# Optimization experiments

Hardware: AMD Instinct MI355X
Metric: run time of the kernel (lower is better)

The kernel has to match this reference:

```python
import jax, jax.numpy as jnp
import numpy as np

N_ENT = 100000
N_REL = 237
IN_DIM = 128
OUT_DIM = 128
E = 400000


def setup_inputs() -> dict:
    key = jax.random.key(0)
    k1, k2, k3, k4, k5, k6, k7, k8 = jax.random.split(key, 8)
    src = jax.random.randint(k1, (E,), 0, N_ENT)
    dst = jax.random.randint(k2, (E,), 0, N_ENT)
    rel = jax.random.randint(k3, (E,), 0, N_REL)
    triplets = jnp.stack([src, dst, rel], axis=1)  # [E, 3]
    ent_embed = jax.random.normal(k4, (N_ENT, IN_DIM), dtype=jnp.float32)
    rel_embed = jax.random.normal(k5, (N_REL, IN_DIM), dtype=jnp.float32)
    # xavier_normal with gain=1.414 for weights; torch Linear bias ~ U(-1/sqrt(fan_in), 1/sqrt(fan_in))
    g = 1.414
    Wa = jax.random.normal(k6, (OUT_DIM, 3 * IN_DIM), dtype=jnp.float32) * (g * np.sqrt(2.0 / (3 * IN_DIM + OUT_DIM)))
    ba = jnp.zeros((OUT_DIM,), dtype=jnp.float32)
    Wa2 = jax.random.normal(k7, (1, OUT_DIM), dtype=jnp.float32) * (g * np.sqrt(2.0 / (OUT_DIM + 1)))
    ba2 = jnp.zeros((1,), dtype=jnp.float32)
    return {"triplets": triplets, "ent_embed": ent_embed, "rel_embed": rel_embed,
            "Wa": Wa, "ba": ba, "Wa2": Wa2, "ba2": ba2}


def reference(triplets, ent_embed, rel_embed, Wa, ba, Wa2, ba2):
    src, dst, rel = triplets[:, 0], triplets[:, 1], triplets[:, 2]
    # per-edge feature: [E, 3*in_dim]
    h = jnp.concatenate([ent_embed[src], rel_embed[rel], ent_embed[dst]], axis=1)
    c = h @ Wa.T + ba                                  # [E, out_dim]
    b = jax.nn.leaky_relu(c @ Wa2.T + ba2)             # [E, 1], slope 0.01
    e_b = jnp.exp(b)                                   # [E, 1]
    # segment-sum over source nodes (torch.sparse.sum over dim=1 of [N,N,F])
    e_b_sum = jax.ops.segment_sum(e_b, src, num_segments=N_ENT)       # [N, 1]
    temp1 = e_b * c                                    # [E, out_dim]
    h_sum = jax.ops.segment_sum(temp1, src, num_segments=N_ENT)       # [N, out_dim]
    ebs = jnp.where(e_b_sum == 0, 1e-12, e_b_sum)
    h_ent = h_sum / ebs                                # [N, out_dim]
    # scatter-mean of temp1 by relation id
    rel_sum = jax.ops.segment_sum(temp1, rel, num_segments=N_REL)     # [R, out_dim]
    rel_cnt = jax.ops.segment_sum(jnp.ones((temp1.shape[0], 1), temp1.dtype), rel, num_segments=N_REL)
    h_rel = rel_sum / jnp.maximum(rel_cnt, 1.0)        # [R, out_dim]
    return jax.nn.elu(h_ent), jax.nn.elu(h_rel)
```

## Files before the change

### kernel.cpp

```cpp
#include <hip/hip_runtime.h>
#include <math.h>

#define N_ENT 100000
#define N_REL 237
#define DIM   128
#define NE    400000


__global__ void k_transpose_wa(const float* __restrict__ Wa, float* __restrict__ WaT) {
    int i = blockIdx.x * 256 + threadIdx.x;
    if (i < 384 * 128) {
        int k = i >> 7, j = i & 127;
        WaT[i] = Wa[j * 384 + k];
    }
}

__global__ void k_proj_rel(const float* __restrict__ rel_e, const float* __restrict__ Wa,
                           const float* __restrict__ ba, float* __restrict__ Pr) {
    int i = blockIdx.x * 256 + threadIdx.x;
    if (i >= N_REL * DIM) return;
    int r = i >> 7, j = i & 127;
    float acc = ba[j];
    const float* wrow = Wa + j * 384 + 128;
    const float* erow = rel_e + r * DIM;
    #pragma unroll 8
    for (int k = 0; k < DIM; ++k) acc += erow[k] * wrow[k];
    Pr[i] = acc;
}

#define KC 16
__global__ __launch_bounds__(256) void k_proj_ent(const float* __restrict__ ent,
        const float* __restrict__ WaT, float* __restrict__ Ps, float* __restrict__ Pd) {
    __shared__ float tile[64 * 132];
    __shared__ float wsh[2 * KC * 128];
    const int tid = threadIdx.x;
    const int row0 = blockIdx.x * 64;

    for (int i = tid; i < 64 * 32; i += 256) {
        int r = i >> 5, c4 = i & 31;
        float4 v = make_float4(0.f, 0.f, 0.f, 0.f);
        if (row0 + r < N_ENT) v = *(const float4*)(ent + (size_t)(row0 + r) * DIM + c4 * 4);
        *(float4*)(tile + r * 132 + c4 * 4) = v;
    }

    const int rg = tid >> 4, cg = tid & 15;
    const int r0 = rg * 4, j0 = cg * 8;

    float accs[4][8], accd[4][8];
    #pragma unroll
    for (int i = 0; i < 4; ++i)
        #pragma unroll
        for (int j = 0; j < 8; ++j) { accs[i][j] = 0.f; accd[i][j] = 0.f; }

    for (int kc = 0; kc < DIM; kc += KC) {
        __syncthreads();
        for (int i = tid; i < KC * 32; i += 256) {
            int kk = i >> 5, c4 = i & 31;
            *(float4*)(wsh + kk * 128 + c4 * 4) =
                *(const float4*)(WaT + (kc + kk) * 128 + c4 * 4);
            *(float4*)(wsh + KC * 128 + kk * 128 + c4 * 4) =
                *(const float4*)(WaT + (256 + kc + kk) * 128 + c4 * 4);
        }
        __syncthreads();
        #pragma unroll
        for (int kk = 0; kk < KC; ++kk) {
            float4 a0 = *(float4*)(wsh + kk * 128 + j0);
            float4 a1 = *(float4*)(wsh + kk * 128 + j0 + 4);
            float4 b0 = *(float4*)(wsh + KC * 128 + kk * 128 + j0);
            float4 b1 = *(float4*)(wsh + KC * 128 + kk * 128 + j0 + 4);
            float ws[8] = {a0.x, a0.y, a0.z, a0.w, a1.x, a1.y, a1.z, a1.w};
            float wd[8] = {b0.x, b0.y, b0.z, b0.w, b1.x, b1.y, b1.z, b1.w};
            #pragma unroll
            for (int i = 0; i < 4; ++i) {
                float e = tile[(r0 + i) * 132 + kc + kk];
                #pragma unroll
                for (int j = 0; j < 8; ++j) {
                    accs[i][j] += e * ws[j];
                    accd[i][j] += e * wd[j];
                }
            }
        }
    }

    #pragma unroll
    for (int i = 0; i < 4; ++i) {
        int row = row0 + r0 + i;
        if (row < N_ENT) {
            float4 o;
            o = make_float4(accs[i][0], accs[i][1], accs[i][2], accs[i][3]);
            *(float4*)(Ps + (size_t)row * DIM + j0) = o;
            o = make_float4(accs[i][4], accs[i][5], accs[i][6], accs[i][7]);
            *(float4*)(Ps + (size_t)row * DIM + j0 + 4) = o;
            o = make_float4(accd[i][0], accd[i][1], accd[i][2], accd[i][3]);
            *(float4*)(Pd + (size_t)row * DIM + j0) = o;
            o = make_float4(accd[i][4], accd[i][5], accd[i][6], accd[i][7]);
            *(float4*)(Pd + (size_t)row * DIM + j0 + 4) = o;
        }
    }
}

__global__ void k_hist2(const int* __restrict__ trip, int* __restrict__ scnt,
                        int* __restrict__ rcnt) {
    __shared__ int lh[N_REL];
    for (int i = threadIdx.x; i < N_REL; i += 256) lh[i] = 0;
    __syncthreads();
    int e0 = blockIdx.x * 1024 + threadIdx.x * 4;
    #pragma unroll
    for (int k = 0; k < 4; ++k) {
        int e = e0 + k;
        if (e < NE) {
            atomicAdd(scnt + trip[3 * e], 1);
            atomicAdd(&lh[trip[3 * e + 2]], 1);
        }
    }
    __syncthreads();
    for (int i = threadIdx.x; i < N_REL; i += 256)
        if (lh[i]) atomicAdd(rcnt + i, lh[i]);
}

__global__ void k_scan1(const int* __restrict__ cnt, int* __restrict__ escan,
                        int* __restrict__ bsum) {
    __shared__ int sh[256];
    const int t = threadIdx.x;
    int base = blockIdx.x * 1024 + t * 4;
    int v[4]; int s = 0;
    #pragma unroll
    for (int k = 0; k < 4; ++k) { int idx = base + k; v[k] = (idx < N_ENT) ? cnt[idx] : 0; s += v[k]; }
    sh[t] = s; __syncthreads();
    for (int off = 1; off < 256; off <<= 1) {
        int u = (t >= off) ? sh[t - off] : 0;
        __syncthreads();
        sh[t] += u;
        __syncthreads();
    }
    int run = sh[t] - s;
    #pragma unroll
    for (int k = 0; k < 4; ++k) { int idx = base + k; if (idx < N_ENT) escan[idx] = run; run += v[k]; }
    if (t == 255) bsum[blockIdx.x] = sh[255];
}

__global__ void k_scan2(int* __restrict__ bsum) {
    __shared__ int sh[128];
    const int t = threadIdx.x;
    int v = (t < 98) ? bsum[t] : 0;
    sh[t] = v; __syncthreads();
    for (int off = 1; off < 128; off <<= 1) {
        int u = (t >= off) ? sh[t - off] : 0;
        __syncthreads();
        sh[t] += u;
        __syncthreads();
    }
    if (t < 98) bsum[t] = sh[t] - v;
}

__global__ void k_scan3(int* __restrict__ row_start, const int* __restrict__ bsum,
                        int* __restrict__ cursor) {
    int i = blockIdx.x * 256 + threadIdx.x;
    if (i < N_ENT) {
        int v = row_start[i] + bsum[i >> 10];
        row_start[i] = v;
        cursor[i] = v;
    } else if (i == N_ENT) {
        row_start[N_ENT] = NE;
    }
}

__global__ void k_relscan(const int* __restrict__ rcnt, int* __restrict__ rrow,
                          int* __restrict__ rcursor) {
    __shared__ int sh[256];
    const int t = threadIdx.x;
    int v = (t < N_REL) ? rcnt[t] : 0;
    sh[t] = v; __syncthreads();
    for (int off = 1; off < 256; off <<= 1) {
        int u = (t >= off) ? sh[t - off] : 0;
        __syncthreads();
        sh[t] += u;
        __syncthreads();
    }
    int excl = sh[t] - v;
    if (t <= N_REL) rrow[t] = excl;
    if (t < N_REL) rcursor[t] = excl;
}

__global__ __launch_bounds__(256) void k_scatter3(const int* __restrict__ trip,
        int* __restrict__ scursor, int* __restrict__ rcursor,
        int* __restrict__ sdst, int* __restrict__ srel,
        int* __restrict__ rsrc, int* __restrict__ rdst) {
    __shared__ int lh[N_REL];
    __shared__ int lbase[N_REL];
    const int t = threadIdx.x;
    for (int i = t; i < N_REL; i += 256) lh[i] = 0;
    __syncthreads();

    const int e0 = blockIdx.x * 1024 + t * 4;
    int sv[4], dv[4], rv[4];
    #pragma unroll
    for (int k = 0; k < 4; ++k) {
        int e = e0 + k;
        if (e < NE) {
            sv[k] = trip[3 * e]; dv[k] = trip[3 * e + 1]; rv[k] = trip[3 * e + 2];
            atomicAdd(&lh[rv[k]], 1);
        } else { sv[k] = -1; }
    }
    __syncthreads();
    for (int i = t; i < N_REL; i += 256) {
        int c = lh[i];
        lbase[i] = c ? atomicAdd(rcursor + i, c) : 0;
        lh[i] = 0;
    }
    __syncthreads();
    #pragma unroll
    for (int k = 0; k < 4; ++k) {
        if (sv[k] >= 0) {
            int p1 = atomicAdd(scursor + sv[k], 1);
            sdst[p1] = dv[k];
            srel[p1] = rv[k];
            int intra = atomicAdd(&lh[rv[k]], 1);
            int p2 = lbase[rv[k]] + intra;
            rsrc[p2] = sv[k];
            rdst[p2] = dv[k];
        }
    }
}

__global__ __launch_bounds__(256) void k_seg(const int* __restrict__ row_start,
        const int* __restrict__ sdst, const int* __restrict__ srel,
        const float* __restrict__ Ps, const float* __restrict__ Pd, const float* __restrict__ Pr,
        const float* __restrict__ Wa2, const float* __restrict__ ba2,
        float* __restrict__ out) {
    const int lane = threadIdx.x & 63;
    const int s = (blockIdx.x * 256 + threadIdx.x) >> 6;
    if (s >= N_ENT) return;
    const float w0 = Wa2[lane], w1 = Wa2[64 + lane];
    const float bb = ba2[0];

    const int beg = row_start[s], end = row_start[s + 1];
    const float ps0 = Ps[(size_t)s * DIM + lane];
    const float ps1 = Ps[(size_t)s * DIM + 64 + lane];

    float acc0 = 0.f, acc1 = 0.f, ebs = 0.f;
    for (int j = beg; j < end; ++j) {
        int d = sdst[j];
        int r = srel[j];
        float c0 = ps0 + Pr[r * DIM + lane]      + Pd[(size_t)d * DIM + lane];
        float c1 = ps1 + Pr[r * DIM + 64 + lane] + Pd[(size_t)d * DIM + 64 + lane];
        float p = c0 * w0 + c1 * w1;
        #pragma unroll
        for (int off = 32; off > 0; off >>= 1) p += __shfl_xor(p, off, 64);
        float b = p + bb;
        b = (b > 0.f) ? b : 0.01f * b;
        float eb = expf(b);
        acc0 += eb * c0; acc1 += eb * c1; ebs += eb;
    }

    float ebsv = (ebs == 0.f) ? 1e-12f : ebs;
    float h0 = acc0 / ebsv, h1 = acc1 / ebsv;
    out[(size_t)s * DIM + lane]      = (h0 > 0.f) ? h0 : expm1f(h0);
    out[(size_t)s * DIM + 64 + lane] = (h1 > 0.f) ? h1 : expm1f(h1);
}

__global__ __launch_bounds__(1024) void k_relseg2(const int* __restrict__ rrow,
        const int* __restrict__ rcnt,
        const int* __restrict__ rsrc, const int* __restrict__ rdst,
        const float* __restrict__ Ps, const float* __restrict__ Pd, const float* __restrict__ Pr,
        const float* __restrict__ Wa2, const float* __restrict__ ba2,
        float* __restrict__ out) {
    __shared__ float red[16 * 128];
    const int r = blockIdx.x;
    const int t = threadIdx.x;
    const int lane = t & 63;
    const int w = t >> 6;
    const float w0 = Wa2[lane], w1 = Wa2[64 + lane];
    const float bb = ba2[0];

    const int beg = rrow[r], end = rrow[r + 1];
    const float pr0 = Pr[r * DIM + lane];
    const float pr1 = Pr[r * DIM + 64 + lane];

    float a0 = 0.f, a1 = 0.f;
    for (int j = beg + w; j < end; j += 16) {
        int s = rsrc[j], d = rdst[j];
        float c0 = pr0 + Ps[(size_t)s * DIM + lane]      + Pd[(size_t)d * DIM + lane];
        float c1 = pr1 + Ps[(size_t)s * DIM + 64 + lane] + Pd[(size_t)d * DIM + 64 + lane];
        float p = c0 * w0 + c1 * w1;
        #pragma unroll
        for (int off = 32; off > 0; off >>= 1) p += __shfl_xor(p, off, 64);
        float b = p + bb;
        b = (b > 0.f) ? b : 0.01f * b;
        float eb = expf(b);
        a0 += eb * c0; a1 += eb * c1;
    }
    red[w * 128 + lane]      = a0;
    red[w * 128 + 64 + lane] = a1;
    __syncthreads();
    if (t < 128) {
        float s = 0.f;
        #pragma unroll
        for (int ww = 0; ww < 16; ++ww) s += red[ww * 128 + t];
        float h = s / fmaxf((float)rcnt[r], 1.0f);
        out[(size_t)N_ENT * DIM + r * DIM + t] = (h > 0.f) ? h : expm1f(h);
    }
}

extern "C" void kernel_launch(void* const* d_in, const int* in_sizes, int n_in,
                              void* d_out, int out_size, void* d_ws, size_t ws_size,
                              hipStream_t stream) {
    const int*   trip = (const int*)d_in[0];
    const float* ent  = (const float*)d_in[1];
    const float* rele = (const float*)d_in[2];
    const float* Wa   = (const float*)d_in[3];
    const float* ba   = (const float*)d_in[4];
    const float* Wa2  = (const float*)d_in[5];
    const float* ba2  = (const float*)d_in[6];
    float* out = (float*)d_out;

    float* ws  = (float*)d_ws;
    float* WaT = ws;
    float* Ps  = WaT + 384 * 128;
    float* Pd  = Ps + (size_t)N_ENT * DIM;
    float* Pr  = Pd + (size_t)N_ENT * DIM;
    int* row_start = (int*)(Pr + N_REL * DIM);
    int* cursor    = row_start + N_ENT + 1;
    int* rcnt      = cursor + N_ENT;
    int* rrow      = rcnt + 240;
    int* rcursor   = rrow + 240;
    int* bsum      = rcursor + 240;
    int* sdst      = bsum + 128;
    int* srel      = sdst + NE;
    int* rsrc      = srel + NE;
    int* rdst      = rsrc + NE;

    hipMemsetAsync(cursor, 0, (N_ENT + 240) * sizeof(int), stream);

    k_transpose_wa<<<192, 256, 0, stream>>>(Wa, WaT);
    k_proj_rel<<<(N_REL * DIM + 255) / 256, 256, 0, stream>>>(rele, Wa, ba, Pr);
    k_proj_ent<<<(N_ENT + 63) / 64, 256, 0, stream>>>(ent, WaT, Ps, Pd);

    k_hist2<<<(NE + 1023) / 1024, 256, 0, stream>>>(trip, cursor, rcnt);
    k_scan1<<<98, 256, 0, stream>>>(cursor, row_start, bsum);
    k_scan2<<<1, 128, 0, stream>>>(bsum);
    k_scan3<<<(N_ENT + 256) / 256, 256, 0, stream>>>(row_start, bsum, cursor);
    k_relscan<<<1, 256, 0, stream>>>(rcnt, rrow, rcursor);
    k_scatter3<<<(NE + 1023) / 1024, 256, 0, stream>>>(trip, cursor, rcursor,
                                                       sdst, srel, rsrc, rdst);

    k_seg<<<(N_ENT + 3) / 4, 256, 0, stream>>>(row_start, sdst, srel, Ps, Pd, Pr,
                                               Wa2, ba2, out);
    k_relseg2<<<N_REL, 1024, 0, stream>>>(rrow, rcnt, rsrc, rdst, Ps, Pd, Pr,
                                          Wa2, ba2, out);
}
```

Measured before the change: 459.8 us.

## Precompute per-node attention logits and pack edge index arrays

Uses linearity of the attention score to precompute scalar projections qs, qd, qr (Wa2 dotted with the source, destination and relation projections). Each edge's logit then becomes three scalar loads instead of a wave-wide reduction. The constant source term is moved out of the segment accumulation, and the relation mean adds Pr scaled by the exp-sum. Edge index arrays are packed into int2, and the entity GEMM now reads entity rows directly from global memory instead of a shared tile, with a permuted weight layout. Risks include slightly different floating-point summation order and uncoalesced global reads of entity rows in the GEMM.

```diff
diff --git a/kernel.cpp b/kernel.cpp
--- a/kernel.cpp
+++ b/kernel.cpp
@@ -28,23 +28,34 @@
     Pr[i] = acc;
 }
 
+__global__ void k_qr(const float* __restrict__ Pr, const float* __restrict__ Wa2,
+                     const float* __restrict__ ba2, float* __restrict__ qr) {
+    const int lane = threadIdx.x & 63;
+    const int r = (blockIdx.x * 256 + threadIdx.x) >> 6;
+    if (r >= N_REL) return;
+    float p = Pr[r * DIM + lane] * Wa2[lane] + Pr[r * DIM + 64 + lane] * Wa2[64 + lane];
+    #pragma unroll
+    for (int off = 32; off > 0; off >>= 1) p += __shfl_xor(p, off, 64);
+    if (lane == 0) qr[r] = p + ba2[0];
+}
+
 #define KC 16
 __global__ __launch_bounds__(256) void k_proj_ent(const float* __restrict__ ent,
-        const float* __restrict__ WaT, float* __restrict__ Ps, float* __restrict__ Pd) {
-    __shared__ float tile[64 * 132];
-    __shared__ float wsh[2 * KC * 128];
+        const float* __restrict__ WaT, const float* __restrict__ Wa2,
+        float* __restrict__ Ps, float* __restrict__ Pd,
+        float* __restrict__ qs, float* __restrict__ qd) {
+    __shared__ float wsh[2 * KC * 132];
     const int tid = threadIdx.x;
     const int row0 = blockIdx.x * 64;
-
-    for (int i = tid; i < 64 * 32; i += 256) {
-        int r = i >> 5, c4 = i & 31;
-        float4 v = make_float4(0.f, 0.f, 0.f, 0.f);
-        if (row0 + r < N_ENT) v = *(const float4*)(ent + (size_t)(row0 + r) * DIM + c4 * 4);
-        *(float4*)(tile + r * 132 + c4 * 4) = v;
-    }
-
     const int rg = tid >> 4, cg = tid & 15;
     const int r0 = rg * 4, j0 = cg * 8;
+
+    int rows[4];
+    #pragma unroll
+    for (int i = 0; i < 4; ++i) {
+        int rr = row0 + r0 + i;
+        rows[i] = (rr < N_ENT) ? rr : (N_ENT - 1);
+    }
 
     float accs[4][8], accd[4][8];
     #pragma unroll
@@ -53,30 +64,42 @@
         for (int j = 0; j < 8; ++j) { accs[i][j] = 0.f; accd[i][j] = 0.f; }
 
     for (int kc = 0; kc < DIM; kc += KC) {
-        __syncthreads();
-        for (int i = tid; i < KC * 32; i += 256) {
-            int kk = i >> 5, c4 = i & 31;
-            *(float4*)(wsh + kk * 128 + c4 * 4) =
-                *(const float4*)(WaT + (kc + kk) * 128 + c4 * 4);
-            *(float4*)(wsh + KC * 128 + kk * 128 + c4 * 4) =
-                *(const float4*)(WaT + (256 + kc + kk) * 128 + c4 * 4);
-        }
-        __syncthreads();
+        if (kc) __syncthreads();
+        for (int u = tid; u < 2 * KC * 32; u += 256) {
+            int m   = u >> 9;
+            int rem = u & 511;
+            int kk  = rem >> 5, c4 = rem & 31;
+            float4 v = *(const float4*)(WaT + (size_t)((m ? 256 : 0) + kc + kk) * 128 + c4 * 4);
+            int perm = (c4 >> 1) + (c4 & 1) * 16;
+            *(float4*)(wsh + m * KC * 132 + kk * 132 + perm * 4) = v;
+        }
+        __syncthreads();
+
         #pragma unroll
-        for (int kk = 0; kk < KC; ++kk) {
-            float4 a0 = *(float4*)(wsh + kk * 128 + j0);
-            float4 a1 = *(float4*)(wsh + kk * 128 + j0 + 4);
-            float4 b0 = *(float4*)(wsh + KC * 128 + kk * 128 + j0);
-            float4 b1 = *(float4*)(wsh + KC * 128 + kk * 128 + j0 + 4);
-            float ws[8] = {a0.x, a0.y, a0.z, a0.w, a1.x, a1.y, a1.z, a1.w};
-            float wd[8] = {b0.x, b0.y, b0.z, b0.w, b1.x, b1.y, b1.z, b1.w};
+        for (int kq = 0; kq < 4; ++kq) {
+            float ev[4][4];
             #pragma unroll
             for (int i = 0; i < 4; ++i) {
-                float e = tile[(r0 + i) * 132 + kc + kk];
+                float4 t = *(const float4*)(ent + (size_t)rows[i] * DIM + kc + kq * 4);
+                ev[i][0] = t.x; ev[i][1] = t.y; ev[i][2] = t.z; ev[i][3] = t.w;
+            }
+            #pragma unroll
+            for (int kk2 = 0; kk2 < 4; ++kk2) {
+                int kk = kq * 4 + kk2;
+                float4 a0 = *(float4*)(wsh + kk * 132 + cg * 4);
+                float4 a1 = *(float4*)(wsh + kk * 132 + 64 + cg * 4);
+                float4 b0 = *(float4*)(wsh + KC * 132 + kk * 132 + cg * 4);
+                float4 b1 = *(float4*)(wsh + KC * 132 + kk * 132 + 64 + cg * 4);
+                float ws[8] = {a0.x, a0.y, a0.z, a0.w, a1.x, a1.y, a1.z, a1.w};
+                float wd[8] = {b0.x, b0.y, b0.z, b0.w, b1.x, b1.y, b1.z, b1.w};
                 #pragma unroll
-                for (int j = 0; j < 8; ++j) {
-                    accs[i][j] += e * ws[j];
-                    accd[i][j] += e * wd[j];
+                for (int i = 0; i < 4; ++i) {
+                    float e = ev[i][kk2];
+                    #pragma unroll
+                    for (int j = 0; j < 8; ++j) {
+                        accs[i][j] += e * ws[j];
+                        accd[i][j] += e * wd[j];
+                    }
                 }
             }
         }
@@ -97,6 +120,33 @@
             *(float4*)(Pd + (size_t)row * DIM + j0 + 4) = o;
         }
     }
+
+    __syncthreads();
+    float4 w2a = *(const float4*)(Wa2 + j0);
+    float4 w2b = *(const float4*)(Wa2 + j0 + 4);
+    float w2v[8] = {w2a.x, w2a.y, w2a.z, w2a.w, w2b.x, w2b.y, w2b.z, w2b.w};
+    #pragma unroll
+    for (int i = 0; i < 4; ++i) {
+        float p_s = 0.f, p_d = 0.f;
+        #pragma unroll
+        for (int j = 0; j < 8; ++j) { p_s += accs[i][j] * w2v[j]; p_d += accd[i][j] * w2v[j]; }
+        wsh[(r0 + i) * 16 + cg]        = p_s;
+        wsh[1024 + (r0 + i) * 16 + cg] = p_d;
+    }
+    __syncthreads();
+    if (tid < 64) {
+        int row = row0 + tid;
+        if (row < N_ENT) {
+            float ss = 0.f, sd = 0.f;
+            #pragma unroll
+            for (int c = 0; c < 16; ++c) {
+                ss += wsh[tid * 16 + c];
+                sd += wsh[1024 + tid * 16 + c];
+            }
+            qs[row] = ss;
+            qd[row] = sd;
+        }
+    }
 }
 
 __global__ void k_hist2(const int* __restrict__ trip, int* __restrict__ scnt,
@@ -184,8 +234,7 @@
 
 __global__ __launch_bounds__(256) void k_scatter3(const int* __restrict__ trip,
         int* __restrict__ scursor, int* __restrict__ rcursor,
-        int* __restrict__ sdst, int* __restrict__ srel,
-        int* __restrict__ rsrc, int* __restrict__ rdst) {
+        int2* __restrict__ sdr, int2* __restrict__ rsd) {
     __shared__ int lh[N_REL];
     __shared__ int lbase[N_REL];
     const int t = threadIdx.x;
@@ -213,91 +262,78 @@
     for (int k = 0; k < 4; ++k) {
         if (sv[k] >= 0) {
             int p1 = atomicAdd(scursor + sv[k], 1);
-            sdst[p1] = dv[k];
-            srel[p1] = rv[k];
+            sdr[p1] = make_int2(dv[k], rv[k]);
             int intra = atomicAdd(&lh[rv[k]], 1);
-            int p2 = lbase[rv[k]] + intra;
-            rsrc[p2] = sv[k];
-            rdst[p2] = dv[k];
+            rsd[lbase[rv[k]] + intra] = make_int2(sv[k], dv[k]);
         }
     }
 }
 
 __global__ __launch_bounds__(256) void k_seg(const int* __restrict__ row_start,
-        const int* __restrict__ sdst, const int* __restrict__ srel,
+        const int2* __restrict__ sdr,
         const float* __restrict__ Ps, const float* __restrict__ Pd, const float* __restrict__ Pr,
-        const float* __restrict__ Wa2, const float* __restrict__ ba2,
+        const float* __restrict__ qs, const float* __restrict__ qd, const float* __restrict__ qr,
         float* __restrict__ out) {
     const int lane = threadIdx.x & 63;
     const int s = (blockIdx.x * 256 + threadIdx.x) >> 6;
     if (s >= N_ENT) return;
-    const float w0 = Wa2[lane], w1 = Wa2[64 + lane];
-    const float bb = ba2[0];
 
     const int beg = row_start[s], end = row_start[s + 1];
-    const float ps0 = Ps[(size_t)s * DIM + lane];
-    const float ps1 = Ps[(size_t)s * DIM + 64 + lane];
-
+    if (beg == end) {
+        out[(size_t)s * DIM + lane] = 0.f;
+        out[(size_t)s * DIM + 64 + lane] = 0.f;
+        return;
+    }
+    const float myqs = qs[s];
     float acc0 = 0.f, acc1 = 0.f, ebs = 0.f;
     for (int j = beg; j < end; ++j) {
-        int d = sdst[j];
-        int r = srel[j];
-        float c0 = ps0 + Pr[r * DIM + lane]      + Pd[(size_t)d * DIM + lane];
-        float c1 = ps1 + Pr[r * DIM + 64 + lane] + Pd[(size_t)d * DIM + 64 + lane];
-        float p = c0 * w0 + c1 * w1;
-        #pragma unroll
-        for (int off = 32; off > 0; off >>= 1) p += __shfl_xor(p, off, 64);
-        float b = p + bb;
+        int2 dr = sdr[j];
+        float b = myqs + qr[dr.y] + qd[dr.x];
         b = (b > 0.f) ? b : 0.01f * b;
         float eb = expf(b);
-        acc0 += eb * c0; acc1 += eb * c1; ebs += eb;
-    }
-
-    float ebsv = (ebs == 0.f) ? 1e-12f : ebs;
-    float h0 = acc0 / ebsv, h1 = acc1 / ebsv;
+        acc0 += eb * (Pr[dr.y * DIM + lane]      + Pd[(size_t)dr.x * DIM + lane]);
+        acc1 += eb * (Pr[dr.y * DIM + 64 + lane] + Pd[(size_t)dr.x * DIM + 64 + lane]);
+        ebs += eb;
+    }
+    float h0 = Ps[(size_t)s * DIM + lane]      + acc0 / ebs;
+    float h1 = Ps[(size_t)s * DIM + 64 + lane] + acc1 / ebs;
     out[(size_t)s * DIM + lane]      = (h0 > 0.f) ? h0 : expm1f(h0);
     out[(size_t)s * DIM + 64 + lane] = (h1 > 0.f) ? h1 : expm1f(h1);
 }
 
 __global__ __launch_bounds__(1024) void k_relseg2(const int* __restrict__ rrow,
-        const int* __restrict__ rcnt,
-        const int* __restrict__ rsrc, const int* __restrict__ rdst,
+        const int2* __restrict__ rsd,
         const float* __restrict__ Ps, const float* __restrict__ Pd, const float* __restrict__ Pr,
-        const float* __restrict__ Wa2, const float* __restrict__ ba2,
+        const float* __restrict__ qs, const float* __restrict__ qd, const float* __restrict__ qr,
         float* __restrict__ out) {
     __shared__ float red[16 * 128];
+    __shared__ float reb[16];
     const int r = blockIdx.x;
     const int t = threadIdx.x;
     const int lane = t & 63;
     const int w = t >> 6;
-    const float w0 = Wa2[lane], w1 = Wa2[64 + lane];
-    const float bb = ba2[0];
+    const float myqr = qr[r];
 
     const int beg = rrow[r], end = rrow[r + 1];
-    const float pr0 = Pr[r * DIM + lane];
-    const float pr1 = Pr[r * DIM + 64 + lane];
-
-    float a0 = 0.f, a1 = 0.f;
+    float a0 = 0.f, a1 = 0.f, ebs = 0.f;
     for (int j = beg + w; j < end; j += 16) {
-        int s = rsrc[j], d = rdst[j];
-        float c0 = pr0 + Ps[(size_t)s * DIM + lane]      + Pd[(size_t)d * DIM + lane];
-        float c1 = pr1 + Ps[(size_t)s * DIM + 64 + lane] + Pd[(size_t)d * DIM + 64 + lane];
-        float p = c0 * w0 + c1 * w1;
-        #pragma unroll
-        for (int off = 32; off > 0; off >>= 1) p += __shfl_xor(p, off, 64);
-        float b = p + bb;
+        int2 sd = rsd[j];
+        float b = myqr + qs[sd.x] + qd[sd.y];
         b = (b > 0.f) ? b : 0.01f * b;
         float eb = expf(b);
-        a0 += eb * c0; a1 += eb * c1;
+        a0 += eb * (Ps[(size_t)sd.x * DIM + lane]      + Pd[(size_t)sd.y * DIM + lane]);
+        a1 += eb * (Ps[(size_t)sd.x * DIM + 64 + lane] + Pd[(size_t)sd.y * DIM + 64 + lane]);
+        ebs += eb;
     }
     red[w * 128 + lane]      = a0;
     red[w * 128 + 64 + lane] = a1;
+    if (lane == 0) reb[w] = ebs;
     __syncthreads();
     if (t < 128) {
-        float s = 0.f;
+        float ssum = 0.f, et = 0.f;
         #pragma unroll
-        for (int ww = 0; ww < 16; ++ww) s += red[ww * 128 + t];
-        float h = s / fmaxf((float)rcnt[r], 1.0f);
+        for (int ww = 0; ww < 16; ++ww) { ssum += red[ww * 128 + t]; et += reb[ww]; }
+        float h = (ssum + et * Pr[r * DIM + t]) / fmaxf((float)(end - beg), 1.0f);
         out[(size_t)N_ENT * DIM + r * DIM + t] = (h > 0.f) ? h : expm1f(h);
     }
 }
@@ -319,33 +355,33 @@
     float* Ps  = WaT + 384 * 128;
     float* Pd  = Ps + (size_t)N_ENT * DIM;
     float* Pr  = Pd + (size_t)N_ENT * DIM;
-    int* row_start = (int*)(Pr + N_REL * DIM);
+    float* qs  = Pr + N_REL * DIM;
+    float* qd  = qs + N_ENT;
+    float* qr  = qd + N_ENT;
+    int* row_start = (int*)(qr + 240);
     int* cursor    = row_start + N_ENT + 1;
     int* rcnt      = cursor + N_ENT;
     int* rrow      = rcnt + 240;
     int* rcursor   = rrow + 240;
     int* bsum      = rcursor + 240;
-    int* sdst      = bsum + 128;
-    int* srel      = sdst + NE;
-    int* rsrc      = srel + NE;
-    int* rdst      = rsrc + NE;
+    int2* sdr      = (int2*)(bsum + 128);
+    int2* rsd      = sdr + NE;
 
     hipMemsetAsync(cursor, 0, (N_ENT + 240) * sizeof(int), stream);
 
     k_transpose_wa<<<192, 256, 0, stream>>>(Wa, WaT);
     k_proj_rel<<<(N_REL * DIM + 255) / 256, 256, 0, stream>>>(rele, Wa, ba, Pr);
-    k_proj_ent<<<(N_ENT + 63) / 64, 256, 0, stream>>>(ent, WaT, Ps, Pd);
+    k_qr<<<(N_REL * 64 + 255) / 256, 256, 0, stream>>>(Pr, Wa2, ba2, qr);
+    k_proj_ent<<<(N_ENT + 63) / 64, 256, 0, stream>>>(ent, WaT, Wa2, Ps, Pd, qs, qd);
 
     k_hist2<<<(NE + 1023) / 1024, 256, 0, stream>>>(trip, cursor, rcnt);
     k_scan1<<<98, 256, 0, stream>>>(cursor, row_start, bsum);
     k_scan2<<<1, 128, 0, stream>>>(bsum);
     k_scan3<<<(N_ENT + 256) / 256, 256, 0, stream>>>(row_start, bsum, cursor);
     k_relscan<<<1, 256, 0, stream>>>(rcnt, rrow, rcursor);
-    k_scatter3<<<(NE + 1023) / 1024, 256, 0, stream>>>(trip, cursor, rcursor,
-                                                       sdst, srel, rsrc, rdst);
-
-    k_seg<<<(N_ENT + 3) / 4, 256, 0, stream>>>(row_start, sdst, srel, Ps, Pd, Pr,
-                                               Wa2, ba2, out);
-    k_relseg2<<<N_REL, 1024, 0, stream>>>(rrow, rcnt, rsrc, rdst, Ps, Pd, Pr,
-                                          Wa2, ba2, out);
-}
+    k_scatter3<<<(NE + 1023) / 1024, 256, 0, stream>>>(trip, cursor, rcursor, sdr, rsd);
+
+    k_seg<<<(N_ENT + 3) / 4, 256, 0, stream>>>(row_start, sdr, Ps, Pd, Pr,
+                                               qs, qd, qr, out);
+    k_relseg2<<<N_REL, 1024, 0, stream>>>(rrow, rsd, Ps, Pd, Pr, qs, qd, qr, out);
+}
```

Measured after the change: 432.9 us. 1.06x faster.
